# Kernel tuning notes

Hardware: AMD Instinct MI355X
Metric: run time of the kernel (lower is better)

The kernel has to match this reference:

```python
import jax, jax.numpy as jnp
import numpy as np

B, S, D = 2, 2048, 1024
H, DH = 16, 64  # num_heads, attention_dim


def setup_inputs() -> dict:
    key = jax.random.key(0)
    ks = jax.random.split(key, 10)
    x = jax.random.normal(ks[0], (B, S, D), dtype=jnp.float32)
    # causal mask, broadcast over batch and heads (mask==0 -> -inf)
    mask = jnp.tril(jnp.ones((S, S), dtype=jnp.int32))[None, None]
    s = 1.0 / np.sqrt(D)
    Wq = jax.random.normal(ks[1], (D, H * DH), dtype=jnp.float32) * s
    bq = jnp.zeros((H * DH,), dtype=jnp.float32)
    Wk = jax.random.normal(ks[2], (D, H * DH), dtype=jnp.float32) * s
    bk = jnp.zeros((H * DH,), dtype=jnp.float32)
    Wv = jax.random.normal(ks[3], (D, H * DH), dtype=jnp.float32) * s
    bv = jnp.zeros((H * DH,), dtype=jnp.float32)
    Wo = jax.random.normal(ks[4], (H * DH, D), dtype=jnp.float32) * (1.0 / np.sqrt(H * DH))
    bo = jnp.zeros((D,), dtype=jnp.float32)
    return {"x": x, "mask": mask, "Wq": Wq, "bq": bq, "Wk": Wk, "bk": bk,
            "Wv": Wv, "bv": bv, "Wo": Wo, "bo": bo}


def reference(x, mask, Wq, bq, Wk, bk, Wv, bv, Wo, bo):
    b, s, _ = x.shape
    q = (x @ Wq + bq).reshape(b, s, H, DH)
    k = (x @ Wk + bk).reshape(b, s, H, DH)
    v = (x @ Wv + bv).reshape(b, s, H, DH)
    # scores: [B, H, S, S]
    scores = jnp.einsum("bshd,bthd->bhst", q, k) / jnp.sqrt(jnp.float32(DH))
    scores = jnp.where(mask == 0, -jnp.inf, scores)
    w = jax.nn.softmax(scores, axis=-1)
    attended = jnp.einsum("bhst,bthd->bshd", w, v).reshape(b, s, H * DH)
    return attended @ Wo + bo
```

## Files before the change

kernel.cpp:

```cpp
#include <hip/hip_runtime.h>
#include <hip/hip_bf16.h>

#define B_ 2
#define S_ 2048
#define D_ 1024
#define H_ 16
#define DH_ 64

typedef __attribute__((ext_vector_type(8))) short bf16x8;
typedef __attribute__((ext_vector_type(4))) float f32x4;

#define QSCALE 0.18033688011112042f

__device__ __forceinline__ ushort f2b(float f){
  __hip_bfloat16 h = __float2bfloat16(f);
  return *reinterpret_cast<ushort*>(&h);
}

__device__ __forceinline__ unsigned cvtpk(float lo, float hi){
  unsigned r;
  asm("v_cvt_pk_bf16_f32 %0, %1, %2" : "=v"(r) : "v"(lo), "v"(hi));
  return r;
}

__device__ __forceinline__ void gload16(const ushort* g, ushort* l){
  __builtin_amdgcn_global_load_lds((const __attribute__((address_space(1))) unsigned*)g,
                                   (__attribute__((address_space(3))) unsigned*)l, 16, 0, 0);
}

__global__ __launch_bounds__(256) void k_prep(const float* __restrict__ x, ushort* __restrict__ xb,
                                              const float* __restrict__ Wq, const float* __restrict__ Wk,
                                              const float* __restrict__ Wv, const float* __restrict__ Wo,
                                              ushort* __restrict__ WqkvT, ushort* __restrict__ WoT){
  int bid = blockIdx.x, tid = threadIdx.x;
  if (bid < 2048){
    int i = (bid*256 + tid)*8;
    float4 v0 = *(const float4*)(x + i);
    float4 v1 = *(const float4*)(x + i + 4);
    uint4 o;
    o.x = f2b(v0.x) | ((unsigned)f2b(v0.y)<<16);
    o.y = f2b(v0.z) | ((unsigned)f2b(v0.w)<<16);
    o.z = f2b(v1.x) | ((unsigned)f2b(v1.y)<<16);
    o.w = f2b(v1.z) | ((unsigned)f2b(v1.w)<<16);
    *(uint4*)(xb + i) = o;
    return;
  }
  bid -= 2048;
  const int w = bid >> 10, tb = bid & 1023;
  const float* src = (w==0)?Wq:(w==1)?Wk:(w==2)?Wv:Wo;
  ushort* dst = (w==3)?WoT : WqkvT + (size_t)w*(1024*1024);
  __shared__ float tile[32][33];
  const int bx2 = tb & 31, by2 = tb >> 5;
  const int c0 = bx2*32, r0 = by2*32;
  const int tx = tid & 31, ty = tid >> 5;
  #pragma unroll
  for (int i=0;i<4;i++)
    tile[ty + i*8][tx] = src[(size_t)(r0 + ty + i*8)*1024 + c0 + tx];
  __syncthreads();
  #pragma unroll
  for (int i=0;i<4;i++)
    dst[(size_t)(c0 + ty + i*8)*1024 + r0 + tx] = f2b(tile[tx][ty + i*8]);
}

__global__ __launch_bounds__(512, 4) void k_gemm_qkv(const ushort* __restrict__ A,
                                                     const ushort* __restrict__ BT,
                                                     const float* __restrict__ b0p,
                                                     const float* __restrict__ b1p,
                                                     const float* __restrict__ b2p,
                                                     ushort* __restrict__ Cp,
                                                     int M, int N, int K){
  __shared__ ushort As[256*64];
  __shared__ ushort Bs[128*64];
  const int tid = threadIdx.x;
  const int nbn = N >> 7;
  const int bm = blockIdx.x / nbn, bn = blockIdx.x % nbn;
  const int m0 = bm << 8, n0 = bn << 7;
  const int wave = tid >> 6, lane = tid & 63;
  const int wm = (wave >> 1) << 6, wn = (wave & 1) << 6;
  const int lr = lane & 15, lq = lane >> 4;

  f32x4 acc[4][4] = {};

  const int r0 = tid >> 3;
  const int gk = (tid & 7) ^ (r0 & 7);
  const ushort* Agb = A  + (size_t)(m0 + r0)*K + gk*8;
  const ushort* Bgb = BT + (size_t)(n0 + r0)*K + gk*8;
  const int lofs = tid*8;

  for (int kt = 0; kt < K; kt += 64){
    __syncthreads();
    #pragma unroll
    for (int j=0;j<4;j++)
      gload16(Agb + (size_t)j*64*K + kt, &As[lofs + j*4096]);
    #pragma unroll
    for (int j=0;j<2;j++)
      gload16(Bgb + (size_t)j*64*K + kt, &Bs[lofs + j*4096]);
    __syncthreads();
    #pragma unroll
    for (int kk=0;kk<2;kk++){
      bf16x8 af[4], bfr[4];
      #pragma unroll
      for (int i=0;i<4;i++){
        int ra = wm + i*16 + lr;
        af[i]  = *(bf16x8*)&As[ra*64 + (((kk*4+lq) ^ (ra & 7)) << 3)];
        int rb = wn + i*16 + lr;
        bfr[i] = *(bf16x8*)&Bs[rb*64 + (((kk*4+lq) ^ (rb & 7)) << 3)];
      }
      __builtin_amdgcn_s_setprio(1);
      #pragma unroll
      for (int mi=0;mi<4;mi++)
        #pragma unroll
        for (int ni=0;ni<4;ni++)
          acc[mi][ni] = __builtin_amdgcn_mfma_f32_16x16x32_bf16(af[mi], bfr[ni], acc[mi][ni], 0, 0, 0);
      __builtin_amdgcn_s_setprio(0);
    }
  }

  const int seg = n0 >> 10;
  const float* bp = (seg==0 ? b0p : (seg==1 ? b1p : b2p));
  #pragma unroll
  for (int mi=0;mi<4;mi++){
    #pragma unroll
    for (int ni=0;ni<4;ni++){
      int col = n0 + wn + ni*16 + lr;
      int cl = col & 1023;
      float bv = bp[cl];
      int row0 = m0 + wm + mi*16 + lq*4;
      ushort* Qb = Cp;
      if (seg == 0){
        #pragma unroll
        for (int r=0;r<4;r++)
          Qb[(size_t)(row0+r)*1024 + cl] = f2b((acc[mi][ni][r] + bv) * QSCALE);
      } else if (seg == 1){
        ushort* Kb = Qb + (4u<<20);
        #pragma unroll
        for (int r=0;r<4;r++)
          Kb[(size_t)(row0+r)*1024 + cl] = f2b(acc[mi][ni][r] + bv);
      } else {
        ushort* Vt = Qb + (8u<<20);
        int bb = row0 >> 11, srow = row0 & 2047;
        uint2 pk;
        pk.x = cvtpk(acc[mi][ni][0]+bv, acc[mi][ni][1]+bv);
        pk.y = cvtpk(acc[mi][ni][2]+bv, acc[mi][ni][3]+bv);
        *(uint2*)&Vt[((size_t)(bb*1024 + cl))*2048 + srow] = pk;
      }
    }
  }
}

__global__ __launch_bounds__(256) void k_gemm_out(const ushort* __restrict__ A,
                                                  const ushort* __restrict__ BT,
                                                  const float* __restrict__ bias,
                                                  float* __restrict__ Cp,
                                                  int M, int N, int K){
  __shared__ ushort As[128*64];
  __shared__ ushort Bs[128*64];
  const int tid = threadIdx.x;
  const int nbn = N >> 7;
  const int bm = blockIdx.x / nbn, bn = blockIdx.x % nbn;
  const int m0 = bm << 7, n0 = bn << 7;
  const int wave = tid >> 6, lane = tid & 63;
  const int wm = (wave >> 1) << 6, wn = (wave & 1) << 6;
  const int lr = lane & 15, lq = lane >> 4;

  f32x4 acc[4][4] = {};

  const ushort* Ag[4]; const ushort* Bg[4]; int lofs[4];
  #pragma unroll
  for (int j=0;j<4;j++){
    int c = tid + j*256, row = c >> 3, slot = c & 7;
    int gk2 = slot ^ (row & 7);
    Ag[j] = A  + (size_t)(m0 + row)*K + gk2*8;
    Bg[j] = BT + (size_t)(n0 + row)*K + gk2*8;
    lofs[j] = c*8;
  }

  for (int kt = 0; kt < K; kt += 64){
    __syncthreads();
    #pragma unroll
    for (int j=0;j<4;j++){
      gload16(Ag[j] + kt, &As[lofs[j]]);
      gload16(Bg[j] + kt, &Bs[lofs[j]]);
    }
    __syncthreads();
    #pragma unroll
    for (int kk=0;kk<2;kk++){
      bf16x8 af[4], bfr[4];
      #pragma unroll
      for (int i=0;i<4;i++){
        int ra = wm + i*16 + lr;
        af[i]  = *(bf16x8*)&As[ra*64 + (((kk*4+lq) ^ (ra & 7)) << 3)];
        int rb = wn + i*16 + lr;
        bfr[i] = *(bf16x8*)&Bs[rb*64 + (((kk*4+lq) ^ (rb & 7)) << 3)];
      }
      __builtin_amdgcn_s_setprio(1);
      #pragma unroll
      for (int mi=0;mi<4;mi++)
        #pragma unroll
        for (int ni=0;ni<4;ni++)
          acc[mi][ni] = __builtin_amdgcn_mfma_f32_16x16x32_bf16(af[mi], bfr[ni], acc[mi][ni], 0, 0, 0);
      __builtin_amdgcn_s_setprio(0);
    }
  }

  #pragma unroll
  for (int mi=0;mi<4;mi++){
    #pragma unroll
    for (int ni=0;ni<4;ni++){
      int col = n0 + wn + ni*16 + lr;
      float bv = bias[col];
      int row0 = m0 + wm + mi*16 + lq*4;
      #pragma unroll
      for (int r=0;r<4;r++)
        Cp[(size_t)(row0+r)*N + col] = acc[mi][ni][r] + bv;
    }
  }
}

__device__ __forceinline__ bf16x8 lds_frag(const ushort* base, int row, int colbytes){
  return *(const bf16x8*)((const char*)base + row*128 + (colbytes ^ ((row & 7) << 4)));
}

__global__ __launch_bounds__(256) void k_attn_mfma(const ushort* __restrict__ Qb,
                                                   const ushort* __restrict__ Kb,
                                                   const ushort* __restrict__ Vtg,
                                                   ushort* __restrict__ Ob,
                                                   ushort* __restrict__ accPb,
                                                   float* __restrict__ lP){
  __shared__ ushort Ks[2][64*64];
  __shared__ ushort Vs[2][64*64];
  __shared__ ushort Ps[4][16*64];
  const int bid = blockIdx.x;
  int bh, qt, t0, NT, half; bool split;
  if (bid < 1024){
    int s = bid >> 5; bh = bid & 31;
    qt = 31 - (s >> 1); half = s & 1; split = true;
    if (half == 0){ t0 = 16; NT = qt; }
    else          { t0 = 0;  NT = 15; }
  } else {
    int s = bid - 1024; qt = 15 - (s >> 5); bh = s & 31;
    t0 = 0; NT = qt; half = 0; split = false;
  }
  const bool diag = (!split) || (half == 0);
  const int h = bh & 15, b = bh >> 4;
  const int q0 = qt << 6;
  const int tid = threadIdx.x;
  const int wq = tid >> 6, lane = tid & 63;
  const int ql = lane & 15, g = lane >> 4;

  bf16x8 Qf0, Qf1;
  {
    const ushort* qp = Qb + (size_t)(b*S_ + q0 + wq*16 + ql)*1024 + h*64 + g*8;
    Qf0 = *(const bf16x8*)(qp);
    Qf1 = *(const bf16x8*)(qp + 32);
  }
  bf16x8 ones;
  #pragma unroll
  for (int i=0;i<8;i++) ones[i] = (short)0x3F80;

  f32x4 lsum = {};
  f32x4 acc[4] = {};

  const int r0c = tid >> 3, cc = tid & 7;
  const int r1c = r0c + 32;
  const int gk0 = cc ^ (r0c & 7);
  const int gk1 = cc ^ (r1c & 7);
  const ushort* Kp0 = Kb  + (size_t)(b*S_ + r0c)*1024 + h*64 + gk0*8;
  const ushort* Kp1 = Kb  + (size_t)(b*S_ + r1c)*1024 + h*64 + gk1*8;
  const ushort* Vp0 = Vtg + (size_t)(bh*64 + r0c)*2048 + gk0*8;
  const ushort* Vp1 = Vtg + (size_t)(bh*64 + r1c)*2048 + gk1*8;
  const int lo0 = tid*8, lo1 = tid*8 + 2048;

  #define ASTAGE(t, buf) { \
    gload16(Kp0 + (size_t)(t)*65536, &Ks[buf][lo0]); \
    gload16(Kp1 + (size_t)(t)*65536, &Ks[buf][lo1]); \
    gload16(Vp0 + (t)*64, &Vs[buf][lo0]); \
    gload16(Vp1 + (t)*64, &Vs[buf][lo1]); }

  char* Pb = (char*)Ps + wq*2048;

  ASTAGE(t0, 0);
  __syncthreads();
  int cur = 0;
  for (int kt = t0; ; ++kt){
    if (kt < NT) ASTAGE(kt+1, cur^1);

    f32x4 sf[4] = {};
    __builtin_amdgcn_s_setprio(1);
    #pragma unroll
    for (int ki=0; ki<4; ++ki){
      bf16x8 kf = lds_frag(Ks[cur], ki*16 + ql, g*16);
      sf[ki] = __builtin_amdgcn_mfma_f32_16x16x32_bf16(kf, Qf0, sf[ki], 0, 0, 0);
    }
    #pragma unroll
    for (int ki=0; ki<4; ++ki){
      bf16x8 kf = lds_frag(Ks[cur], ki*16 + ql, 64 + g*16);
      sf[ki] = __builtin_amdgcn_mfma_f32_16x16x32_bf16(kf, Qf1, sf[ki], 0, 0, 0);
    }
    __builtin_amdgcn_s_setprio(0);

    float s[16];
    #pragma unroll
    for (int ki=0; ki<4; ++ki)
      #pragma unroll
      for (int r=0; r<4; ++r)
        s[ki*4+r] = sf[ki][r];
    if (diag && kt == NT){
      const int th = q0 + wq*16 + ql - NT*64;
      #pragma unroll
      for (int ki=0; ki<4; ++ki)
        #pragma unroll
        for (int r=0; r<4; ++r)
          if (ki*16 + g*4 + r > th) s[ki*4+r] = -1e30f;
    }
    #pragma unroll
    for (int i=0; i<16; ++i) s[i] = exp2f(s[i]);

    #pragma unroll
    for (int ki=0; ki<4; ++ki){
      uint2 uu;
      uu.x = cvtpk(s[ki*4+0], s[ki*4+1]);
      uu.y = cvtpk(s[ki*4+2], s[ki*4+3]);
      *(uint2*)(Pb + ql*128 + ((ki*32 + g*8) ^ ((ql & 7) << 4))) = uu;
    }

    __builtin_amdgcn_s_setprio(1);
    #pragma unroll
    for (int ks=0; ks<2; ++ks){
      bf16x8 pf = *(const bf16x8*)(Pb + ql*128 + ((ks*64 + g*16) ^ ((ql & 7) << 4)));
      #pragma unroll
      for (int ni=0; ni<4; ++ni){
        bf16x8 vf = lds_frag(Vs[cur], ni*16 + ql, ks*64 + g*16);
        acc[ni] = __builtin_amdgcn_mfma_f32_16x16x32_bf16(pf, vf, acc[ni], 0, 0, 0);
      }
      lsum = __builtin_amdgcn_mfma_f32_16x16x32_bf16(pf, ones, lsum, 0, 0, 0);
    }
    __builtin_amdgcn_s_setprio(0);

    if (kt == NT) break;
    __syncthreads();
    cur ^= 1;
  }
  #undef ASTAGE

  if (!split){
    ushort* Op = Ob + (size_t)(b*S_ + q0 + wq*16)*1024 + h*64;
    #pragma unroll
    for (int r=0; r<4; ++r){
      float ir = 1.0f / lsum[r];
      #pragma unroll
      for (int ni=0; ni<4; ++ni)
        Op[(size_t)(g*4 + r)*1024 + ni*16 + ql] = f2b(acc[ni][r] * ir);
    }
  } else {
    const int slot = (qt - 16)*32 + bh;
    const int rbase = half*32768 + slot*64 + wq*16;
    #pragma unroll
    for (int r=0; r<4; ++r){
      const int tr = rbase + g*4 + r;
      float ir = 1.0f / lsum[r];
      #pragma unroll
      for (int ni=0; ni<4; ++ni)
        accPb[(size_t)tr*64 + ni*16 + ql] = f2b(acc[ni][r] * ir);
      if (ql == 0) lP[tr] = lsum[r];
    }
  }
}

__global__ __launch_bounds__(256) void k_combine(const ushort* __restrict__ accPb,
                                                 const float* __restrict__ lP,
                                                 ushort* __restrict__ Ob){
  const int slot = blockIdx.x;
  const int qt = 16 + (slot >> 5), bh = slot & 31;
  const int b = bh >> 4, h = bh & 15;
  const int row = threadIdx.x >> 2, dq = (threadIdx.x & 3) * 16;
  const int trA = slot*64 + row, trB = 32768 + slot*64 + row;
  float lA = lP[trA], lB = lP[trB];
  float inv = 1.0f / (lA + lB);
  float wA = lA * inv, wB = lB * inv;
  const ushort* pa = accPb + (size_t)trA*64 + dq;
  const ushort* pb = accPb + (size_t)trB*64 + dq;
  uint4 a0 = *(const uint4*)pa, a1 = *(const uint4*)(pa + 8);
  uint4 b0 = *(const uint4*)pb, b1 = *(const uint4*)(pb + 8);
  unsigned aw[8] = {a0.x,a0.y,a0.z,a0.w,a1.x,a1.y,a1.z,a1.w};
  unsigned bw[8] = {b0.x,b0.y,b0.z,b0.w,b1.x,b1.y,b1.z,b1.w};
  unsigned ow[8];
  #pragma unroll
  for (int e=0;e<8;e++){
    float alo = __uint_as_float(aw[e] << 16), ahi = __uint_as_float(aw[e] & 0xffff0000u);
    float blo = __uint_as_float(bw[e] << 16), bhi = __uint_as_float(bw[e] & 0xffff0000u);
    ow[e] = cvtpk(alo*wA + blo*wB, ahi*wA + bhi*wB);
  }
  ushort* op = Ob + (size_t)(b*S_ + qt*64 + row)*1024 + h*64 + dq;
  uint4 o0, o1;
  o0.x=ow[0]; o0.y=ow[1]; o0.z=ow[2]; o0.w=ow[3];
  o1.x=ow[4]; o1.y=ow[5]; o1.z=ow[6]; o1.w=ow[7];
  *(uint4*)(op)     = o0;
  *(uint4*)(op + 8) = o1;
}

extern "C" void kernel_launch(void* const* d_in, const int* in_sizes, int n_in,
                              void* d_out, int out_size, void* d_ws, size_t ws_size,
                              hipStream_t stream){
  const float* x  = (const float*)d_in[0];
  const float* Wq = (const float*)d_in[2];
  const float* bq = (const float*)d_in[3];
  const float* Wk = (const float*)d_in[4];
  const float* bk = (const float*)d_in[5];
  const float* Wv = (const float*)d_in[6];
  const float* bv = (const float*)d_in[7];
  const float* Wo = (const float*)d_in[8];
  const float* bo = (const float*)d_in[9];

  char* ws = (char*)d_ws;
  const size_t MB = 1024u*1024u;
  ushort* xb    = (ushort*)(ws + 0);
  ushort* WqkvT = (ushort*)(ws + 8*MB);
  ushort* WoT   = (ushort*)(ws + 14*MB);
  ushort* Qb    = (ushort*)(ws + 16*MB);
  ushort* Kb    = (ushort*)(ws + 24*MB);
  ushort* Vtg   = (ushort*)(ws + 32*MB);
  float*  lP    = (float*)(ws + 40*MB);
  ushort* attb  = xb;
  ushort* accPb = (ushort*)d_out;

  const int MN = B_*S_;

  k_prep<<<dim3(6144), dim3(256), 0, stream>>>(x, xb, Wq, Wk, Wv, Wo, WqkvT, WoT);

  k_gemm_qkv<<<dim3((MN/256)*(3072/128)), dim3(512), 0, stream>>>(xb, WqkvT, bq, bk, bv, Qb, MN, 3072, 1024);

  k_attn_mfma<<<dim3(1536), dim3(256), 0, stream>>>(Qb, Kb, Vtg, attb, accPb, lP);
  k_combine<<<dim3(512), dim3(256), 0, stream>>>(accPb, lP, attb);

  k_gemm_out<<<dim3((MN/128)*(1024/128)), dim3(256), 0, stream>>>(attb, WoT, bo, (float*)d_out, MN, 1024, 1024);
}
```

Before: 111.1 us.

## Double attention query tile to 128 rows per block to reuse K/V loads

Each attention block now handles 128 query rows (two 16-row MFMA sub-tiles per wave) instead of 64, so every K/V tile staged in LDS feeds twice as many MFMAs. The split-KV scheduling, causal mask handling and combine kernel are remapped for the 128-row tiles, halving grid sizes. The aim is to cut global and LDS traffic per unit of compute. In exchange it doubles accumulator registers, which may lower occupancy, and it coarsens the load balance across CUs.

```diff
diff --git a/kernel.cpp b/kernel.cpp
--- a/kernel.cpp
+++ b/kernel.cpp
@@ -229,37 +229,40 @@
                                                    float* __restrict__ lP){
   __shared__ ushort Ks[2][64*64];
   __shared__ ushort Vs[2][64*64];
-  __shared__ ushort Ps[4][16*64];
+  __shared__ ushort Ps[4][2][16*64];
   const int bid = blockIdx.x;
-  int bh, qt, t0, NT, half; bool split;
-  if (bid < 1024){
+  int bh, qb, t0, NT, half; bool split;
+  if (bid < 512){
     int s = bid >> 5; bh = bid & 31;
-    qt = 31 - (s >> 1); half = s & 1; split = true;
-    if (half == 0){ t0 = 16; NT = qt; }
-    else          { t0 = 0;  NT = 15; }
+    qb = 15 - (s >> 1); half = s & 1; split = true;
+    if (half == 0){ t0 = 0;      NT = qb; }
+    else          { t0 = qb + 1; NT = 2*qb + 1; }
   } else {
-    int s = bid - 1024; qt = 15 - (s >> 5); bh = s & 31;
-    t0 = 0; NT = qt; half = 0; split = false;
-  }
-  const bool diag = (!split) || (half == 0);
+    int s = bid - 512; qb = 7 - (s >> 5); bh = s & 31;
+    t0 = 0; NT = 2*qb + 1; half = 0; split = false;
+  }
+  const bool diag = (!split) || (half == 1);
   const int h = bh & 15, b = bh >> 4;
-  const int q0 = qt << 6;
+  const int q0 = qb << 7;
   const int tid = threadIdx.x;
   const int wq = tid >> 6, lane = tid & 63;
   const int ql = lane & 15, g = lane >> 4;
 
-  bf16x8 Qf0, Qf1;
+  bf16x8 Qf0a, Qf0b, Qf1a, Qf1b;
   {
-    const ushort* qp = Qb + (size_t)(b*S_ + q0 + wq*16 + ql)*1024 + h*64 + g*8;
-    Qf0 = *(const bf16x8*)(qp);
-    Qf1 = *(const bf16x8*)(qp + 32);
+    const ushort* qp0 = Qb + (size_t)(b*S_ + q0 + wq*32 + ql)*1024 + h*64 + g*8;
+    Qf0a = *(const bf16x8*)(qp0);
+    Qf0b = *(const bf16x8*)(qp0 + 32);
+    const ushort* qp1 = qp0 + (size_t)16*1024;
+    Qf1a = *(const bf16x8*)(qp1);
+    Qf1b = *(const bf16x8*)(qp1 + 32);
   }
   bf16x8 ones;
   #pragma unroll
   for (int i=0;i<8;i++) ones[i] = (short)0x3F80;
 
-  f32x4 lsum = {};
-  f32x4 acc[4] = {};
+  f32x4 ls0 = {}, ls1 = {};
+  f32x4 acc0[4] = {}, acc1[4] = {};
 
   const int r0c = tid >> 3, cc = tid & 7;
   const int r1c = r0c + 32;
@@ -277,7 +280,8 @@
     gload16(Vp0 + (t)*64, &Vs[buf][lo0]); \
     gload16(Vp1 + (t)*64, &Vs[buf][lo1]); }
 
-  char* Pb = (char*)Ps + wq*2048;
+  char* Pb0 = (char*)Ps + wq*4096;
+  char* Pb1 = Pb0 + 2048;
 
   ASTAGE(t0, 0);
   __syncthreads();
@@ -285,55 +289,68 @@
   for (int kt = t0; ; ++kt){
     if (kt < NT) ASTAGE(kt+1, cur^1);
 
-    f32x4 sf[4] = {};
+    f32x4 sf0[4] = {}, sf1[4] = {};
     __builtin_amdgcn_s_setprio(1);
     #pragma unroll
     for (int ki=0; ki<4; ++ki){
       bf16x8 kf = lds_frag(Ks[cur], ki*16 + ql, g*16);
-      sf[ki] = __builtin_amdgcn_mfma_f32_16x16x32_bf16(kf, Qf0, sf[ki], 0, 0, 0);
+      sf0[ki] = __builtin_amdgcn_mfma_f32_16x16x32_bf16(kf, Qf0a, sf0[ki], 0, 0, 0);
+      sf1[ki] = __builtin_amdgcn_mfma_f32_16x16x32_bf16(kf, Qf1a, sf1[ki], 0, 0, 0);
     }
     #pragma unroll
     for (int ki=0; ki<4; ++ki){
       bf16x8 kf = lds_frag(Ks[cur], ki*16 + ql, 64 + g*16);
-      sf[ki] = __builtin_amdgcn_mfma_f32_16x16x32_bf16(kf, Qf1, sf[ki], 0, 0, 0);
+      sf0[ki] = __builtin_amdgcn_mfma_f32_16x16x32_bf16(kf, Qf0b, sf0[ki], 0, 0, 0);
+      sf1[ki] = __builtin_amdgcn_mfma_f32_16x16x32_bf16(kf, Qf1b, sf1[ki], 0, 0, 0);
     }
     __builtin_amdgcn_s_setprio(0);
 
-    float s[16];
-    #pragma unroll
-    for (int ki=0; ki<4; ++ki)
-      #pragma unroll
-      for (int r=0; r<4; ++r)
-        s[ki*4+r] = sf[ki][r];
-    if (diag && kt == NT){
-      const int th = q0 + wq*16 + ql - NT*64;
+    const bool dm = diag && (kt >= 2*qb);
+    if (dm){
+      const int th0 = q0 + wq*32 + ql - kt*64;
       #pragma unroll
       for (int ki=0; ki<4; ++ki)
         #pragma unroll
         for (int r=0; r<4; ++r)
-          if (ki*16 + g*4 + r > th) s[ki*4+r] = -1e30f;
-    }
-    #pragma unroll
-    for (int i=0; i<16; ++i) s[i] = exp2f(s[i]);
-
+          if (ki*16 + g*4 + r > th0) sf0[ki][r] = -1e30f;
+    }
     #pragma unroll
     for (int ki=0; ki<4; ++ki){
       uint2 uu;
-      uu.x = cvtpk(s[ki*4+0], s[ki*4+1]);
-      uu.y = cvtpk(s[ki*4+2], s[ki*4+3]);
-      *(uint2*)(Pb + ql*128 + ((ki*32 + g*8) ^ ((ql & 7) << 4))) = uu;
+      uu.x = cvtpk(exp2f(sf0[ki][0]), exp2f(sf0[ki][1]));
+      uu.y = cvtpk(exp2f(sf0[ki][2]), exp2f(sf0[ki][3]));
+      *(uint2*)(Pb0 + ql*128 + ((ki*32 + g*8) ^ ((ql & 7) << 4))) = uu;
+    }
+    if (dm){
+      const int th1 = q0 + wq*32 + 16 + ql - kt*64;
+      #pragma unroll
+      for (int ki=0; ki<4; ++ki)
+        #pragma unroll
+        for (int r=0; r<4; ++r)
+          if (ki*16 + g*4 + r > th1) sf1[ki][r] = -1e30f;
+    }
+    #pragma unroll
+    for (int ki=0; ki<4; ++ki){
+      uint2 uu;
+      uu.x = cvtpk(exp2f(sf1[ki][0]), exp2f(sf1[ki][1]));
+      uu.y = cvtpk(exp2f(sf1[ki][2]), exp2f(sf1[ki][3]));
+      *(uint2*)(Pb1 + ql*128 + ((ki*32 + g*8) ^ ((ql & 7) << 4))) = uu;
     }
 
     __builtin_amdgcn_s_setprio(1);
     #pragma unroll
     for (int ks=0; ks<2; ++ks){
-      bf16x8 pf = *(const bf16x8*)(Pb + ql*128 + ((ks*64 + g*16) ^ ((ql & 7) << 4)));
+      const int pofs = ql*128 + ((ks*64 + g*16) ^ ((ql & 7) << 4));
+      bf16x8 pf0 = *(const bf16x8*)(Pb0 + pofs);
+      bf16x8 pf1 = *(const bf16x8*)(Pb1 + pofs);
       #pragma unroll
       for (int ni=0; ni<4; ++ni){
         bf16x8 vf = lds_frag(Vs[cur], ni*16 + ql, ks*64 + g*16);
-        acc[ni] = __builtin_amdgcn_mfma_f32_16x16x32_bf16(pf, vf, acc[ni], 0, 0, 0);
-      }
-      lsum = __builtin_amdgcn_mfma_f32_16x16x32_bf16(pf, ones, lsum, 0, 0, 0);
+        acc0[ni] = __builtin_amdgcn_mfma_f32_16x16x32_bf16(pf0, vf, acc0[ni], 0, 0, 0);
+        acc1[ni] = __builtin_amdgcn_mfma_f32_16x16x32_bf16(pf1, vf, acc1[ni], 0, 0, 0);
+      }
+      ls0 = __builtin_amdgcn_mfma_f32_16x16x32_bf16(pf0, ones, ls0, 0, 0, 0);
+      ls1 = __builtin_amdgcn_mfma_f32_16x16x32_bf16(pf1, ones, ls1, 0, 0, 0);
     }
     __builtin_amdgcn_s_setprio(0);
 
@@ -344,37 +361,47 @@
   #undef ASTAGE
 
   if (!split){
-    ushort* Op = Ob + (size_t)(b*S_ + q0 + wq*16)*1024 + h*64;
-    #pragma unroll
-    for (int r=0; r<4; ++r){
-      float ir = 1.0f / lsum[r];
-      #pragma unroll
-      for (int ni=0; ni<4; ++ni)
-        Op[(size_t)(g*4 + r)*1024 + ni*16 + ql] = f2b(acc[ni][r] * ir);
+    #pragma unroll
+    for (int u=0; u<2; ++u){
+      ushort* Op = Ob + (size_t)(b*S_ + q0 + wq*32 + u*16)*1024 + h*64;
+      const f32x4* ac = u ? acc1 : acc0;
+      const f32x4& ls = u ? ls1 : ls0;
+      #pragma unroll
+      for (int r=0; r<4; ++r){
+        float ir = 1.0f / ls[r];
+        #pragma unroll
+        for (int ni=0; ni<4; ++ni)
+          Op[(size_t)(g*4 + r)*1024 + ni*16 + ql] = f2b(ac[ni][r] * ir);
+      }
     }
   } else {
-    const int slot = (qt - 16)*32 + bh;
-    const int rbase = half*32768 + slot*64 + wq*16;
-    #pragma unroll
-    for (int r=0; r<4; ++r){
-      const int tr = rbase + g*4 + r;
-      float ir = 1.0f / lsum[r];
-      #pragma unroll
-      for (int ni=0; ni<4; ++ni)
-        accPb[(size_t)tr*64 + ni*16 + ql] = f2b(acc[ni][r] * ir);
-      if (ql == 0) lP[tr] = lsum[r];
-    }
-  }
-}
-
-__global__ __launch_bounds__(256) void k_combine(const ushort* __restrict__ accPb,
+    const int slot = (qb - 8)*32 + bh;
+    #pragma unroll
+    for (int u=0; u<2; ++u){
+      const f32x4* ac = u ? acc1 : acc0;
+      const f32x4& ls = u ? ls1 : ls0;
+      const int rbase = half*32768 + slot*128 + wq*32 + u*16;
+      #pragma unroll
+      for (int r=0; r<4; ++r){
+        const int tr = rbase + g*4 + r;
+        float ir = 1.0f / ls[r];
+        #pragma unroll
+        for (int ni=0; ni<4; ++ni)
+          accPb[(size_t)tr*64 + ni*16 + ql] = f2b(ac[ni][r] * ir);
+        if (ql == 0) lP[tr] = ls[r];
+      }
+    }
+  }
+}
+
+__global__ __launch_bounds__(512) void k_combine(const ushort* __restrict__ accPb,
                                                  const float* __restrict__ lP,
                                                  ushort* __restrict__ Ob){
   const int slot = blockIdx.x;
-  const int qt = 16 + (slot >> 5), bh = slot & 31;
+  const int qb = 8 + (slot >> 5), bh = slot & 31;
   const int b = bh >> 4, h = bh & 15;
   const int row = threadIdx.x >> 2, dq = (threadIdx.x & 3) * 16;
-  const int trA = slot*64 + row, trB = 32768 + slot*64 + row;
+  const int trA = slot*128 + row, trB = 32768 + slot*128 + row;
   float lA = lP[trA], lB = lP[trB];
   float inv = 1.0f / (lA + lB);
   float wA = lA * inv, wB = lB * inv;
@@ -391,7 +418,7 @@
     float blo = __uint_as_float(bw[e] << 16), bhi = __uint_as_float(bw[e] & 0xffff0000u);
     ow[e] = cvtpk(alo*wA + blo*wB, ahi*wA + bhi*wB);
   }
-  ushort* op = Ob + (size_t)(b*S_ + qt*64 + row)*1024 + h*64 + dq;
+  ushort* op = Ob + (size_t)(b*S_ + qb*128 + row)*1024 + h*64 + dq;
   uint4 o0, o1;
   o0.x=ow[0]; o0.y=ow[1]; o0.z=ow[2]; o0.w=ow[3];
   o1.x=ow[4]; o1.y=ow[5]; o1.z=ow[6]; o1.w=ow[7];
@@ -430,8 +457,8 @@
 
   k_gemm_qkv<<<dim3((MN/256)*(3072/128)), dim3(512), 0, stream>>>(xb, WqkvT, bq, bk, bv, Qb, MN, 3072, 1024);
 
-  k_attn_mfma<<<dim3(1536), dim3(256), 0, stream>>>(Qb, Kb, Vtg, attb, accPb, lP);
-  k_combine<<<dim3(512), dim3(256), 0, stream>>>(accPb, lP, attb);
+  k_attn_mfma<<<dim3(768), dim3(256), 0, stream>>>(Qb, Kb, Vtg, attb, accPb, lP);
+  k_combine<<<dim3(256), dim3(512), 0, stream>>>(accPb, lP, attb);
 
   k_gemm_out<<<dim3((MN/128)*(1024/128)), dim3(256), 0, stream>>>(attb, WoT, bo, (float*)d_out, MN, 1024, 1024);
 }
```

Result: slower. 120.1 us (+8.1%).

## Rewrite attention inner loop with 32x32x16 MFMA and register-resident P

Applied to the files above, without the earlier changes.

The attention kernel now uses 2 waves of 128 threads, each owning 32 query rows, and runs 32x32x16 bf16 MFMAs in place of 16x16x32. The probability tile stays in registers and is rearranged into the A-operand layout with cross-half lane shuffles, so the LDS P scratch buffer and its write/read round trip are gone. The row sum is now a plain VALU accumulation instead of an MFMA against a ones vector. This is meant to cut LDS traffic and MFMA issue count, but each block has fewer waves to hide latency and each thread must issue more global-to-LDS loads per stage.

```diff
diff --git a/kernel.cpp b/kernel.cpp
--- a/kernel.cpp
+++ b/kernel.cpp
@@ -9,6 +9,7 @@
 
 typedef __attribute__((ext_vector_type(8))) short bf16x8;
 typedef __attribute__((ext_vector_type(4))) float f32x4;
+typedef __attribute__((ext_vector_type(16))) float f32x16;
 
 #define QSCALE 0.18033688011112042f
 
@@ -217,11 +218,7 @@
   }
 }
 
-__device__ __forceinline__ bf16x8 lds_frag(const ushort* base, int row, int colbytes){
-  return *(const bf16x8*)((const char*)base + row*128 + (colbytes ^ ((row & 7) << 4)));
-}
-
-__global__ __launch_bounds__(256) void k_attn_mfma(const ushort* __restrict__ Qb,
+__global__ __launch_bounds__(128) void k_attn_mfma(const ushort* __restrict__ Qb,
                                                    const ushort* __restrict__ Kb,
                                                    const ushort* __restrict__ Vtg,
                                                    ushort* __restrict__ Ob,
@@ -229,7 +226,6 @@
                                                    float* __restrict__ lP){
   __shared__ ushort Ks[2][64*64];
   __shared__ ushort Vs[2][64*64];
-  __shared__ ushort Ps[4][16*64];
   const int bid = blockIdx.x;
   int bh, qt, t0, NT, half; bool split;
   if (bid < 1024){
@@ -246,38 +242,35 @@
   const int q0 = qt << 6;
   const int tid = threadIdx.x;
   const int wq = tid >> 6, lane = tid & 63;
-  const int ql = lane & 15, g = lane >> 4;
-
-  bf16x8 Qf0, Qf1;
+  const int ql = lane & 31, hi = lane >> 5;
+
+  bf16x8 Qf[4];
   {
-    const ushort* qp = Qb + (size_t)(b*S_ + q0 + wq*16 + ql)*1024 + h*64 + g*8;
-    Qf0 = *(const bf16x8*)(qp);
-    Qf1 = *(const bf16x8*)(qp + 32);
-  }
-  bf16x8 ones;
-  #pragma unroll
-  for (int i=0;i<8;i++) ones[i] = (short)0x3F80;
-
-  f32x4 lsum = {};
-  f32x4 acc[4] = {};
+    const ushort* qp = Qb + (size_t)(b*S_ + q0 + wq*32 + ql)*1024 + h*64 + hi*8;
+    #pragma unroll
+    for (int dc=0; dc<4; ++dc) Qf[dc] = *(const bf16x8*)(qp + dc*16);
+  }
+
+  float lsum = 0.f;
+  f32x16 acc0 = {}, acc1 = {};
 
   const int r0c = tid >> 3, cc = tid & 7;
-  const int r1c = r0c + 32;
-  const int gk0 = cc ^ (r0c & 7);
-  const int gk1 = cc ^ (r1c & 7);
-  const ushort* Kp0 = Kb  + (size_t)(b*S_ + r0c)*1024 + h*64 + gk0*8;
-  const ushort* Kp1 = Kb  + (size_t)(b*S_ + r1c)*1024 + h*64 + gk1*8;
-  const ushort* Vp0 = Vtg + (size_t)(bh*64 + r0c)*2048 + gk0*8;
-  const ushort* Vp1 = Vtg + (size_t)(bh*64 + r1c)*2048 + gk1*8;
-  const int lo0 = tid*8, lo1 = tid*8 + 2048;
+  const int gk = cc ^ (r0c & 7);
+  const ushort* Kp = Kb  + (size_t)(b*S_ + r0c)*1024 + h*64 + gk*8;
+  const ushort* Vp = Vtg + (size_t)(bh*64 + r0c)*2048 + gk*8;
+  const int lofs = tid*8;
 
   #define ASTAGE(t, buf) { \
-    gload16(Kp0 + (size_t)(t)*65536, &Ks[buf][lo0]); \
-    gload16(Kp1 + (size_t)(t)*65536, &Ks[buf][lo1]); \
-    gload16(Vp0 + (t)*64, &Vs[buf][lo0]); \
-    gload16(Vp1 + (t)*64, &Vs[buf][lo1]); }
-
-  char* Pb = (char*)Ps + wq*2048;
+    const ushort* kp_ = Kp + (size_t)(t)*65536; \
+    const ushort* vp_ = Vp + (t)*64; \
+    gload16(kp_,           &Ks[buf][lofs]); \
+    gload16(kp_ + 16*1024, &Ks[buf][lofs+1024]); \
+    gload16(kp_ + 32*1024, &Ks[buf][lofs+2048]); \
+    gload16(kp_ + 48*1024, &Ks[buf][lofs+3072]); \
+    gload16(vp_,           &Vs[buf][lofs]); \
+    gload16(vp_ + 16*2048, &Vs[buf][lofs+1024]); \
+    gload16(vp_ + 32*2048, &Vs[buf][lofs+2048]); \
+    gload16(vp_ + 48*2048, &Vs[buf][lofs+3072]); }
 
   ASTAGE(t0, 0);
   __syncthreads();
@@ -285,57 +278,67 @@
   for (int kt = t0; ; ++kt){
     if (kt < NT) ASTAGE(kt+1, cur^1);
 
-    f32x4 sf[4] = {};
-    __builtin_amdgcn_s_setprio(1);
-    #pragma unroll
-    for (int ki=0; ki<4; ++ki){
-      bf16x8 kf = lds_frag(Ks[cur], ki*16 + ql, g*16);
-      sf[ki] = __builtin_amdgcn_mfma_f32_16x16x32_bf16(kf, Qf0, sf[ki], 0, 0, 0);
-    }
-    #pragma unroll
-    for (int ki=0; ki<4; ++ki){
-      bf16x8 kf = lds_frag(Ks[cur], ki*16 + ql, 64 + g*16);
-      sf[ki] = __builtin_amdgcn_mfma_f32_16x16x32_bf16(kf, Qf1, sf[ki], 0, 0, 0);
-    }
-    __builtin_amdgcn_s_setprio(0);
-
-    float s[16];
-    #pragma unroll
-    for (int ki=0; ki<4; ++ki)
-      #pragma unroll
-      for (int r=0; r<4; ++r)
-        s[ki*4+r] = sf[ki][r];
-    if (diag && kt == NT){
-      const int th = q0 + wq*16 + ql - NT*64;
-      #pragma unroll
-      for (int ki=0; ki<4; ++ki)
-        #pragma unroll
-        for (int r=0; r<4; ++r)
-          if (ki*16 + g*4 + r > th) s[ki*4+r] = -1e30f;
-    }
-    #pragma unroll
-    for (int i=0; i<16; ++i) s[i] = exp2f(s[i]);
-
-    #pragma unroll
-    for (int ki=0; ki<4; ++ki){
-      uint2 uu;
-      uu.x = cvtpk(s[ki*4+0], s[ki*4+1]);
-      uu.y = cvtpk(s[ki*4+2], s[ki*4+3]);
-      *(uint2*)(Pb + ql*128 + ((ki*32 + g*8) ^ ((ql & 7) << 4))) = uu;
-    }
-
-    __builtin_amdgcn_s_setprio(1);
-    #pragma unroll
-    for (int ks=0; ks<2; ++ks){
-      bf16x8 pf = *(const bf16x8*)(Pb + ql*128 + ((ks*64 + g*16) ^ ((ql & 7) << 4)));
-      #pragma unroll
-      for (int ni=0; ni<4; ++ni){
-        bf16x8 vf = lds_frag(Vs[cur], ni*16 + ql, ks*64 + g*16);
-        acc[ni] = __builtin_amdgcn_mfma_f32_16x16x32_bf16(pf, vf, acc[ni], 0, 0, 0);
-      }
-      lsum = __builtin_amdgcn_mfma_f32_16x16x32_bf16(pf, ones, lsum, 0, 0, 0);
-    }
-    __builtin_amdgcn_s_setprio(0);
+    #pragma unroll
+    for (int kg = 0; kg < 2; ++kg){
+      f32x16 sf = {};
+      const int krow = kg*32 + ql;
+      __builtin_amdgcn_s_setprio(1);
+      #pragma unroll
+      for (int dc = 0; dc < 4; ++dc){
+        bf16x8 kf = *(const bf16x8*)((const char*)Ks[cur] + krow*128 + ((dc*32 + hi*16) ^ ((krow & 7) << 4)));
+        sf = __builtin_amdgcn_mfma_f32_32x32x16_bf16(kf, Qf[dc], sf, 0, 0, 0);
+      }
+      __builtin_amdgcn_s_setprio(0);
+
+      float p[16];
+      if (diag && kt == NT){
+        const int th = q0 + wq*32 + ql - kt*64 - kg*32 - 4*hi;
+        #pragma unroll
+        for (int r=0;r<16;++r){
+          int kin = (r&3) + 8*(r>>2);
+          p[r] = exp2f(kin > th ? -1e30f : sf[r]);
+        }
+      } else {
+        #pragma unroll
+        for (int r=0;r<16;++r) p[r] = exp2f(sf[r]);
+      }
+      float s16 = 0.f;
+      #pragma unroll
+      for (int r=0;r<16;++r) s16 += p[r];
+      lsum += s16;
+
+      unsigned w0=cvtpk(p[0],p[1]),   w1=cvtpk(p[2],p[3]);
+      unsigned w2=cvtpk(p[4],p[5]),   w3=cvtpk(p[6],p[7]);
+      unsigned w4=cvtpk(p[8],p[9]),   w5=cvtpk(p[10],p[11]);
+      unsigned w6=cvtpk(p[12],p[13]), w7=cvtpk(p[14],p[15]);
+      unsigned z0 = (unsigned)__shfl_xor((int)(hi ? w0 : w2), 32, 64);
+      unsigned z1 = (unsigned)__shfl_xor((int)(hi ? w1 : w3), 32, 64);
+      unsigned z2 = (unsigned)__shfl_xor((int)(hi ? w4 : w6), 32, 64);
+      unsigned z3 = (unsigned)__shfl_xor((int)(hi ? w5 : w7), 32, 64);
+      uint4 fa, fb;
+      fa.x = hi ? z0 : w0;  fa.y = hi ? z1 : w1;
+      fa.z = hi ? w2 : z0;  fa.w = hi ? w3 : z1;
+      fb.x = hi ? z2 : w4;  fb.y = hi ? z3 : w5;
+      fb.z = hi ? w6 : z2;  fb.w = hi ? w7 : z3;
+      bf16x8 pf0 = *(bf16x8*)&fa;
+      bf16x8 pf1 = *(bf16x8*)&fb;
+
+      __builtin_amdgcn_s_setprio(1);
+      {
+        const char* vbase = (const char*)Vs[cur];
+        const int vr0 = ql;
+        const int vr1 = 32 + ql;
+        bf16x8 v00 = *(const bf16x8*)(vbase + vr0*128 + ((kg*64 + hi*16)      ^ ((vr0 & 7) << 4)));
+        bf16x8 v01 = *(const bf16x8*)(vbase + vr0*128 + ((kg*64 + 32 + hi*16) ^ ((vr0 & 7) << 4)));
+        bf16x8 v10 = *(const bf16x8*)(vbase + vr1*128 + ((kg*64 + hi*16)      ^ ((vr1 & 7) << 4)));
+        bf16x8 v11 = *(const bf16x8*)(vbase + vr1*128 + ((kg*64 + 32 + hi*16) ^ ((vr1 & 7) << 4)));
+        acc0 = __builtin_amdgcn_mfma_f32_32x32x16_bf16(pf0, v00, acc0, 0, 0, 0);
+        acc0 = __builtin_amdgcn_mfma_f32_32x32x16_bf16(pf1, v01, acc0, 0, 0, 0);
+        acc1 = __builtin_amdgcn_mfma_f32_32x32x16_bf16(pf0, v10, acc1, 0, 0, 0);
+        acc1 = __builtin_amdgcn_mfma_f32_32x32x16_bf16(pf1, v11, acc1, 0, 0, 0);
+      }
+      __builtin_amdgcn_s_setprio(0);
+    }
 
     if (kt == NT) break;
     __syncthreads();
@@ -343,27 +346,30 @@
   }
   #undef ASTAGE
 
+  float lst = lsum + __shfl_xor(lsum, 32, 64);
+  float irv = 1.0f / lst;
+
   if (!split){
-    ushort* Op = Ob + (size_t)(b*S_ + q0 + wq*16)*1024 + h*64;
-    #pragma unroll
-    for (int r=0; r<4; ++r){
-      float ir = 1.0f / lsum[r];
-      #pragma unroll
-      for (int ni=0; ni<4; ++ni)
-        Op[(size_t)(g*4 + r)*1024 + ni*16 + ql] = f2b(acc[ni][r] * ir);
+    ushort* Opb = Ob + (size_t)(b*S_)*1024 + h*64;
+    #pragma unroll
+    for (int r=0;r<16;++r){
+      int qr = (r&3) + 8*(r>>2) + 4*hi;
+      float ir = __shfl(irv, qr, 64);
+      size_t row = (size_t)(q0 + wq*32 + qr);
+      Opb[row*1024 + ql]      = f2b(acc0[r] * ir);
+      Opb[row*1024 + 32 + ql] = f2b(acc1[r] * ir);
     }
   } else {
     const int slot = (qt - 16)*32 + bh;
-    const int rbase = half*32768 + slot*64 + wq*16;
-    #pragma unroll
-    for (int r=0; r<4; ++r){
-      const int tr = rbase + g*4 + r;
-      float ir = 1.0f / lsum[r];
-      #pragma unroll
-      for (int ni=0; ni<4; ++ni)
-        accPb[(size_t)tr*64 + ni*16 + ql] = f2b(acc[ni][r] * ir);
-      if (ql == 0) lP[tr] = lsum[r];
-    }
+    const int rb = half*32768 + slot*64 + wq*32;
+    #pragma unroll
+    for (int r=0;r<16;++r){
+      int qr = (r&3) + 8*(r>>2) + 4*hi;
+      float ir = __shfl(irv, qr, 64);
+      accPb[(size_t)(rb + qr)*64 + ql]      = f2b(acc0[r] * ir);
+      accPb[(size_t)(rb + qr)*64 + 32 + ql] = f2b(acc1[r] * ir);
+    }
+    if (lane < 32) lP[rb + ql] = lst;
   }
 }
 
@@ -430,7 +436,7 @@
 
   k_gemm_qkv<<<dim3((MN/256)*(3072/128)), dim3(512), 0, stream>>>(xb, WqkvT, bq, bk, bv, Qb, MN, 3072, 1024);
 
-  k_attn_mfma<<<dim3(1536), dim3(256), 0, stream>>>(Qb, Kb, Vtg, attb, accPb, lP);
+  k_attn_mfma<<<dim3(1536), dim3(128), 0, stream>>>(Qb, Kb, Vtg, attb, accPb, lP);
   k_combine<<<dim3(512), dim3(256), 0, stream>>>(accPb, lP, attb);
 
   k_gemm_out<<<dim3((MN/128)*(1024/128)), dim3(256), 0, stream>>>(attb, WoT, bo, (float*)d_out, MN, 1024, 1024);
```

Measured after the change: 119.8 us. 1.08x slower.

## Replace double-buffered direct-to-LDS K/V loads with register-staged single buffer

Applied to the files above, without the earlier changes.

The attention kernel stops using two LDS buffers filled by direct global-to-LDS loads. It now prefetches the next K/V tile into registers, then writes it to a single swizzled LDS buffer between two barriers at the top of each iteration. This halves K/V LDS usage, which may raise occupancy, and keeps the global prefetch overlapped with compute. In exchange it adds a second barrier per iteration, extra VGPRs and explicit LDS store instructions.

```diff
diff --git a/kernel.cpp b/kernel.cpp
--- a/kernel.cpp
+++ b/kernel.cpp
@@ -227,8 +227,8 @@
                                                    ushort* __restrict__ Ob,
                                                    ushort* __restrict__ accPb,
                                                    float* __restrict__ lP){
-  __shared__ ushort Ks[2][64*64];
-  __shared__ ushort Vs[2][64*64];
+  __shared__ ushort Ks[64*64];
+  __shared__ ushort Vs[64*64];
   __shared__ ushort Ps[4][16*64];
   const int bid = blockIdx.x;
   int bh, qt, t0, NT, half; bool split;
@@ -263,38 +263,42 @@
 
   const int r0c = tid >> 3, cc = tid & 7;
   const int r1c = r0c + 32;
-  const int gk0 = cc ^ (r0c & 7);
-  const int gk1 = cc ^ (r1c & 7);
-  const ushort* Kp0 = Kb  + (size_t)(b*S_ + r0c)*1024 + h*64 + gk0*8;
-  const ushort* Kp1 = Kb  + (size_t)(b*S_ + r1c)*1024 + h*64 + gk1*8;
-  const ushort* Vp0 = Vtg + (size_t)(bh*64 + r0c)*2048 + gk0*8;
-  const ushort* Vp1 = Vtg + (size_t)(bh*64 + r1c)*2048 + gk1*8;
-  const int lo0 = tid*8, lo1 = tid*8 + 2048;
-
-  #define ASTAGE(t, buf) { \
-    gload16(Kp0 + (size_t)(t)*65536, &Ks[buf][lo0]); \
-    gload16(Kp1 + (size_t)(t)*65536, &Ks[buf][lo1]); \
-    gload16(Vp0 + (t)*64, &Vs[buf][lo0]); \
-    gload16(Vp1 + (t)*64, &Vs[buf][lo1]); }
+  const int ofs0 = r0c*128 + ((cc*16) ^ ((r0c & 7) << 4));
+  const int ofs1 = r1c*128 + ((cc*16) ^ ((r1c & 7) << 4));
+  const ushort* Kp0 = Kb  + (size_t)(b*S_ + r0c)*1024 + h*64 + cc*8;
+  const ushort* Kp1 = Kb  + (size_t)(b*S_ + r1c)*1024 + h*64 + cc*8;
+  const ushort* Vp0 = Vtg + (size_t)(bh*64 + r0c)*2048 + cc*8;
+  const ushort* Vp1 = Vtg + (size_t)(bh*64 + r1c)*2048 + cc*8;
+
+  uint4 ka, kc, va, vc;
+  #define ALOAD(t) { \
+    ka = *(const uint4*)(Kp0 + (size_t)(t)*65536); \
+    kc = *(const uint4*)(Kp1 + (size_t)(t)*65536); \
+    va = *(const uint4*)(Vp0 + (t)*64); \
+    vc = *(const uint4*)(Vp1 + (t)*64); }
 
   char* Pb = (char*)Ps + wq*2048;
 
-  ASTAGE(t0, 0);
-  __syncthreads();
-  int cur = 0;
+  ALOAD(t0);
   for (int kt = t0; ; ++kt){
-    if (kt < NT) ASTAGE(kt+1, cur^1);
+    __syncthreads();
+    *(uint4*)((char*)Ks + ofs0) = ka;
+    *(uint4*)((char*)Ks + ofs1) = kc;
+    *(uint4*)((char*)Vs + ofs0) = va;
+    *(uint4*)((char*)Vs + ofs1) = vc;
+    __syncthreads();
+    if (kt < NT) ALOAD(kt+1);
 
     f32x4 sf[4] = {};
     __builtin_amdgcn_s_setprio(1);
     #pragma unroll
     for (int ki=0; ki<4; ++ki){
-      bf16x8 kf = lds_frag(Ks[cur], ki*16 + ql, g*16);
+      bf16x8 kf = lds_frag(Ks, ki*16 + ql, g*16);
       sf[ki] = __builtin_amdgcn_mfma_f32_16x16x32_bf16(kf, Qf0, sf[ki], 0, 0, 0);
     }
     #pragma unroll
     for (int ki=0; ki<4; ++ki){
-      bf16x8 kf = lds_frag(Ks[cur], ki*16 + ql, 64 + g*16);
+      bf16x8 kf = lds_frag(Ks, ki*16 + ql, 64 + g*16);
       sf[ki] = __builtin_amdgcn_mfma_f32_16x16x32_bf16(kf, Qf1, sf[ki], 0, 0, 0);
     }
     __builtin_amdgcn_s_setprio(0);
@@ -330,7 +334,7 @@
       bf16x8 pf = *(const bf16x8*)(Pb + ql*128 + ((ks*64 + g*16) ^ ((ql & 7) << 4)));
       #pragma unroll
       for (int ni=0; ni<4; ++ni){
-        bf16x8 vf = lds_frag(Vs[cur], ni*16 + ql, ks*64 + g*16);
+        bf16x8 vf = lds_frag(Vs, ni*16 + ql, ks*64 + g*16);
         acc[ni] = __builtin_amdgcn_mfma_f32_16x16x32_bf16(pf, vf, acc[ni], 0, 0, 0);
       }
       lsum = __builtin_amdgcn_mfma_f32_16x16x32_bf16(pf, ones, lsum, 0, 0, 0);
@@ -338,10 +342,8 @@
     __builtin_amdgcn_s_setprio(0);
 
     if (kt == NT) break;
-    __syncthreads();
-    cur ^= 1;
-  }
-  #undef ASTAGE
+  }
+  #undef ALOAD
 
   if (!split){
     ushort* Op = Ob + (size_t)(b*S_ + q0 + wq*16)*1024 + h*64;
```

New measurement: 112.5 us. No clear change (+1.2%).
